# Kernel tuning notes

Measured on AMD Instinct MI355X. Metric: run time of the kernel, lower is better.

Reference implementation:

```python
import jax, jax.numpy as jnp
import numpy as np

EPS = 1e-8
TEMP = 0.1

def setup_inputs() -> dict:
    key = jax.random.key(0)
    k1, k2, k3, k4, k5 = jax.random.split(key, 5)
    B, C, S, D = 4096, 1000, 5, 2048
    return {
        "query": jax.random.normal(k1, (B, D), dtype=jnp.float32),
        "labels": jax.random.randint(k2, (B,), 0, C),
        "memory_keys": jax.random.normal(k3, (C, S, D), dtype=jnp.float32),
        "memory_values": jax.random.normal(k4, (C, S, D), dtype=jnp.float32),
        "quality_scores": jax.random.uniform(k5, (C, S), dtype=jnp.float32),
        "top_k": 3,
    }

def reference(query, labels, memory_keys, memory_values, quality_scores, top_k):
    # Gather per-sample class slices: (B, S, D) and (B, S)
    class_keys = memory_keys[labels]
    class_vals = memory_values[labels]
    class_scores = quality_scores[labels]

    # Cosine similarity between query[i] and its class's slot keys
    qn = query / jnp.maximum(jnp.linalg.norm(query, axis=-1, keepdims=True), EPS)
    kn = class_keys / jnp.maximum(jnp.linalg.norm(class_keys, axis=-1, keepdims=True), EPS)
    sim = jnp.einsum('bd,bsd->bs', qn, kn)           # (B, S)
    combined = sim * class_scores                    # (B, S)

    k = min(int(top_k), class_scores.shape[1])
    top_scores, top_idx = jax.lax.top_k(combined, k) # (B, k)
    attn = jax.nn.softmax(top_scores / TEMP, axis=-1)
    top_vals = jnp.take_along_axis(class_vals, top_idx[..., None], axis=1)  # (B, k, D)
    retrieved = jnp.einsum('bk,bkd->bd', attn, top_vals)                    # (B, D)

    # miss handling: classes whose quality scores sum to 0 yield zeros
    hit = class_scores.sum(axis=1) != 0              # (B,)
    retrieved = jnp.where(hit[:, None], retrieved, 0.0)
    weights = jnp.where(hit, top_scores.mean(axis=-1), 0.0)
    return retrieved, weights
```

## Files before the change

kernel.cpp:

```cpp
#include <hip/hip_runtime.h>
#include <math.h>

#define THREADS 256
#define WPB 4
#define NSLOT 5
#define EPSF 1e-8f

template<int N4T>
__global__ __launch_bounds__(THREADS, 4) void mb_wave_kernel(
    const float* __restrict__ query,
    const int*   __restrict__ labels,
    const float* __restrict__ mkeys,
    const float* __restrict__ mvals,
    const float* __restrict__ qscores,
    const int*   __restrict__ topk_p,
    float* __restrict__ out_ret,
    float* __restrict__ out_w,
    int B, int n4_rt)
{
    const int tid  = threadIdx.x;
    const int lane = tid & 63;
    const int wave = tid >> 6;
    const int i    = blockIdx.x * WPB + wave;
    if (i >= B) return;

    const int n4 = (N4T > 0) ? N4T : n4_rt;
    const int c  = labels[i];

    int k = topk_p[0];
    if (k > NSLOT) k = NSLOT;
    if (k < 1) k = 1;

    const float4* q4 = reinterpret_cast<const float4*>(query) + (size_t)i * n4;
    const float4* k4 = reinterpret_cast<const float4*>(mkeys) + (size_t)c * NSLOT * n4;
    const float4* v4 = reinterpret_cast<const float4*>(mvals) + (size_t)c * NSLOT * n4;
    float4*       o4 = reinterpret_cast<float4*>(out_ret) + (size_t)i * n4;

    float qq = 0.f;
    float dot[NSLOT], kk[NSLOT];
#pragma unroll
    for (int s = 0; s < NSLOT; ++s) { dot[s] = 0.f; kk[s] = 0.f; }

    auto body1 = [&](int idx) {
        float4 q = q4[idx];
        qq = fmaf(q.x, q.x, fmaf(q.y, q.y, fmaf(q.z, q.z, fmaf(q.w, q.w, qq))));
#pragma unroll
        for (int s = 0; s < NSLOT; ++s) {
            float4 kv = k4[s * n4 + idx];
            dot[s] = fmaf(q.x, kv.x, fmaf(q.y, kv.y, fmaf(q.z, kv.z, fmaf(q.w, kv.w, dot[s]))));
            kk[s]  = fmaf(kv.x, kv.x, fmaf(kv.y, kv.y, fmaf(kv.z, kv.z, fmaf(kv.w, kv.w, kk[s]))));
        }
    };
    if constexpr (N4T > 0) {
#pragma unroll
        for (int j = 0; j < N4T / 64; ++j) body1(lane + j * 64);
    } else {
        for (int idx = lane; idx < n4; idx += 64) body1(idx);
    }

#pragma unroll
    for (int off = 1; off < 64; off <<= 1) {
        qq += __shfl_xor(qq, off);
#pragma unroll
        for (int s = 0; s < NSLOT; ++s) {
            dot[s] += __shfl_xor(dot[s], off);
            kk[s]  += __shfl_xor(kk[s], off);
        }
    }

    float qn = fmaxf(sqrtf(qq), EPSF);

    float scores[NSLOT];
    float ssum = 0.f;
#pragma unroll
    for (int s = 0; s < NSLOT; ++s) {
        scores[s] = qscores[(size_t)c * NSLOT + s];
        ssum += scores[s];
    }

    float comb[NSLOT];
#pragma unroll
    for (int s = 0; s < NSLOT; ++s) {
        float kn = fmaxf(sqrtf(kk[s]), EPSF);
        comb[s] = (dot[s] / (qn * kn)) * scores[s];
    }

    bool used[NSLOT];
#pragma unroll
    for (int s = 0; s < NSLOT; ++s) used[s] = false;
    float tsc[NSLOT];
    int   tix[NSLOT];
#pragma unroll
    for (int j = 0; j < NSLOT; ++j) {
        if (j < k) {
            float best = -INFINITY;
            int bi = 0;
#pragma unroll
            for (int s = 0; s < NSLOT; ++s) {
                if (!used[s] && comb[s] > best) { best = comb[s]; bi = s; }
            }
            used[bi] = true;
            tsc[j] = best;
            tix[j] = bi;
        }
    }

    const bool hit = (ssum != 0.0f);
    float m = tsc[0];
    float esum = 0.f, wsum = 0.f;
    float a[NSLOT];
#pragma unroll
    for (int j = 0; j < NSLOT; ++j) {
        if (j < k) {
            a[j] = __expf((tsc[j] - m) * 10.0f);
            esum += a[j];
            wsum += tsc[j];
        } else {
            a[j] = 0.f;
        }
    }
    float inv = hit ? (1.0f / esum) : 0.0f;
#pragma unroll
    for (int j = 0; j < NSLOT; ++j) a[j] *= inv;

    if (lane == 0) out_w[i] = hit ? (wsum / (float)k) : 0.0f;

    auto body2 = [&](int idx) {
        float4 acc = make_float4(0.f, 0.f, 0.f, 0.f);
#pragma unroll
        for (int j = 0; j < NSLOT; ++j) {
            if (j < k) {
                float4 v = v4[tix[j] * n4 + idx];
                acc.x = fmaf(a[j], v.x, acc.x);
                acc.y = fmaf(a[j], v.y, acc.y);
                acc.z = fmaf(a[j], v.z, acc.z);
                acc.w = fmaf(a[j], v.w, acc.w);
            }
        }
        o4[idx] = acc;
    };
    if constexpr (N4T > 0) {
#pragma unroll
        for (int j = 0; j < N4T / 64; ++j) body2(lane + j * 64);
    } else {
        for (int idx = lane; idx < n4; idx += 64) body2(idx);
    }
}

extern "C" void kernel_launch(void* const* d_in, const int* in_sizes, int n_in,
                              void* d_out, int out_size, void* d_ws, size_t ws_size,
                              hipStream_t stream) {
    const float* query   = (const float*)d_in[0];
    const int*   labels  = (const int*)d_in[1];
    const float* mkeys   = (const float*)d_in[2];
    const float* mvals   = (const float*)d_in[3];
    const float* qscores = (const float*)d_in[4];
    const int*   topk    = (const int*)d_in[5];

    const int B  = in_sizes[1];
    const int D  = in_sizes[0] / B;
    const int n4 = D >> 2;

    float* out_ret = (float*)d_out;
    float* out_w   = out_ret + (size_t)B * D;

    dim3 grid((B + WPB - 1) / WPB), block(THREADS);
    if (D == 2048) {
        mb_wave_kernel<512><<<grid, block, 0, stream>>>(
            query, labels, mkeys, mvals, qscores, topk, out_ret, out_w, B, n4);
    } else if (D == 1024) {
        mb_wave_kernel<256><<<grid, block, 0, stream>>>(
            query, labels, mkeys, mvals, qscores, topk, out_ret, out_w, B, n4);
    } else {
        mb_wave_kernel<0><<<grid, block, 0, stream>>>(
            query, labels, mkeys, mvals, qscores, topk, out_ret, out_w, B, n4);
    }
}
```

Measured before the change: 49.93 us.

## Software-pipeline key/value loads, use dense slot weights, one wave per block

Restructures the kernel to launch one 64-thread block per query row and adds explicit 3-deep register prefetch of query/key chunks and of value chunks. The top-k attention weights are scattered into a dense per-slot weight vector, so the value phase reads all five slots unconditionally instead of branching on the selected indices. Query loads and output stores use nontemporal hints. This aims to raise memory-level parallelism and remove divergent indexed loads, at the cost of reading two extra value slots per row and higher register pressure.

```diff
diff --git a/kernel.cpp b/kernel.cpp
--- a/kernel.cpp
+++ b/kernel.cpp
@@ -1,13 +1,14 @@
 #include <hip/hip_runtime.h>
 #include <math.h>
 
-#define THREADS 256
-#define WPB 4
 #define NSLOT 5
+#define NBUF 3
 #define EPSF 1e-8f
 
-template<int N4T>
-__global__ __launch_bounds__(THREADS, 4) void mb_wave_kernel(
+typedef float f4 __attribute__((ext_vector_type(4)));
+
+template<int N4>
+__global__ __launch_bounds__(64, 4) void mb_kernel(
     const float* __restrict__ query,
     const int*   __restrict__ labels,
     const float* __restrict__ mkeys,
@@ -18,44 +19,70 @@
     float* __restrict__ out_w,
     int B, int n4_rt)
 {
-    const int tid  = threadIdx.x;
-    const int lane = tid & 63;
-    const int wave = tid >> 6;
-    const int i    = blockIdx.x * WPB + wave;
+    const int lane = threadIdx.x;
+    const int i    = blockIdx.x;
     if (i >= B) return;
-
-    const int n4 = (N4T > 0) ? N4T : n4_rt;
-    const int c  = labels[i];
+    const int c = labels[i];
 
     int k = topk_p[0];
     if (k > NSLOT) k = NSLOT;
     if (k < 1) k = 1;
 
-    const float4* q4 = reinterpret_cast<const float4*>(query) + (size_t)i * n4;
-    const float4* k4 = reinterpret_cast<const float4*>(mkeys) + (size_t)c * NSLOT * n4;
-    const float4* v4 = reinterpret_cast<const float4*>(mvals) + (size_t)c * NSLOT * n4;
-    float4*       o4 = reinterpret_cast<float4*>(out_ret) + (size_t)i * n4;
+    const int n4 = (N4 > 0) ? N4 : n4_rt;
+    const f4* q4 = reinterpret_cast<const f4*>(query) + (size_t)i * n4;
+    const f4* k4 = reinterpret_cast<const f4*>(mkeys) + (size_t)c * NSLOT * n4;
+    const f4* v4 = reinterpret_cast<const f4*>(mvals) + (size_t)c * NSLOT * n4;
+    f4*       o4 = reinterpret_cast<f4*>(out_ret) + (size_t)i * n4;
 
     float qq = 0.f;
     float dot[NSLOT], kk[NSLOT];
 #pragma unroll
     for (int s = 0; s < NSLOT; ++s) { dot[s] = 0.f; kk[s] = 0.f; }
 
-    auto body1 = [&](int idx) {
-        float4 q = q4[idx];
-        qq = fmaf(q.x, q.x, fmaf(q.y, q.y, fmaf(q.z, q.z, fmaf(q.w, q.w, qq))));
-#pragma unroll
-        for (int s = 0; s < NSLOT; ++s) {
-            float4 kv = k4[s * n4 + idx];
-            dot[s] = fmaf(q.x, kv.x, fmaf(q.y, kv.y, fmaf(q.z, kv.z, fmaf(q.w, kv.w, dot[s]))));
-            kk[s]  = fmaf(kv.x, kv.x, fmaf(kv.y, kv.y, fmaf(kv.z, kv.z, fmaf(kv.w, kv.w, kk[s]))));
-        }
-    };
-    if constexpr (N4T > 0) {
-#pragma unroll
-        for (int j = 0; j < N4T / 64; ++j) body1(lane + j * 64);
+    if constexpr (N4 > 0) {
+        constexpr int NCH = N4 / 64;
+        f4 qb[NBUF];
+        f4 kb[NBUF][NSLOT];
+#pragma unroll
+        for (int b = 0; b < NBUF; ++b) {
+            qb[b] = __builtin_nontemporal_load(&q4[lane + b * 64]);
+#pragma unroll
+            for (int s = 0; s < NSLOT; ++s)
+                kb[b][s] = k4[s * N4 + lane + b * 64];
+        }
+#pragma unroll
+        for (int j = 0; j < NCH; ++j) {
+            constexpr int M = NBUF;
+            const int b = j % M;
+            f4 q = qb[b];
+            f4 kv[NSLOT];
+#pragma unroll
+            for (int s = 0; s < NSLOT; ++s) kv[s] = kb[b][s];
+            if (j + M < NCH) {
+                qb[b] = __builtin_nontemporal_load(&q4[lane + (j + M) * 64]);
+#pragma unroll
+                for (int s = 0; s < NSLOT; ++s)
+                    kb[b][s] = k4[s * N4 + lane + (j + M) * 64];
+            }
+            qq = fmaf(q.x, q.x, fmaf(q.y, q.y, fmaf(q.z, q.z, fmaf(q.w, q.w, qq))));
+#pragma unroll
+            for (int s = 0; s < NSLOT; ++s) {
+                dot[s] = fmaf(q.x, kv[s].x, fmaf(q.y, kv[s].y,
+                         fmaf(q.z, kv[s].z, fmaf(q.w, kv[s].w, dot[s]))));
+                kk[s]  = fmaf(kv[s].x, kv[s].x, fmaf(kv[s].y, kv[s].y,
+                         fmaf(kv[s].z, kv[s].z, fmaf(kv[s].w, kv[s].w, kk[s]))));
+            }
+        }
     } else {
-        for (int idx = lane; idx < n4; idx += 64) body1(idx);
+        for (int idx = lane; idx < n4; idx += 64) {
+            f4 q = q4[idx];
+            qq = fmaf(q.x, q.x, fmaf(q.y, q.y, fmaf(q.z, q.z, fmaf(q.w, q.w, qq))));
+            for (int s = 0; s < NSLOT; ++s) {
+                f4 kv = k4[s * n4 + idx];
+                dot[s] = fmaf(q.x, kv.x, fmaf(q.y, kv.y, fmaf(q.z, kv.z, fmaf(q.w, kv.w, dot[s]))));
+                kk[s]  = fmaf(kv.x, kv.x, fmaf(kv.y, kv.y, fmaf(kv.z, kv.z, fmaf(kv.w, kv.w, kk[s]))));
+            }
+        }
     }
 
 #pragma unroll
@@ -92,17 +119,18 @@
     int   tix[NSLOT];
 #pragma unroll
     for (int j = 0; j < NSLOT; ++j) {
+        float best = -INFINITY;
+        int bi = 0;
         if (j < k) {
-            float best = -INFINITY;
-            int bi = 0;
 #pragma unroll
             for (int s = 0; s < NSLOT; ++s) {
                 if (!used[s] && comb[s] > best) { best = comb[s]; bi = s; }
             }
-            used[bi] = true;
-            tsc[j] = best;
-            tix[j] = bi;
-        }
+#pragma unroll
+            for (int s = 0; s < NSLOT; ++s) used[s] = used[s] || (s == bi);
+        }
+        tsc[j] = best;
+        tix[j] = bi;
     }
 
     const bool hit = (ssum != 0.0f);
@@ -120,30 +148,61 @@
         }
     }
     float inv = hit ? (1.0f / esum) : 0.0f;
-#pragma unroll
-    for (int j = 0; j < NSLOT; ++j) a[j] *= inv;
+
+    float w[NSLOT];
+#pragma unroll
+    for (int s = 0; s < NSLOT; ++s) {
+        float ws = 0.f;
+#pragma unroll
+        for (int j = 0; j < NSLOT; ++j)
+            if (j < k && tix[j] == s) ws += a[j] * inv;
+        w[s] = ws;
+    }
 
     if (lane == 0) out_w[i] = hit ? (wsum / (float)k) : 0.0f;
 
-    auto body2 = [&](int idx) {
-        float4 acc = make_float4(0.f, 0.f, 0.f, 0.f);
-#pragma unroll
-        for (int j = 0; j < NSLOT; ++j) {
-            if (j < k) {
-                float4 v = v4[tix[j] * n4 + idx];
-                acc.x = fmaf(a[j], v.x, acc.x);
-                acc.y = fmaf(a[j], v.y, acc.y);
-                acc.z = fmaf(a[j], v.z, acc.z);
-                acc.w = fmaf(a[j], v.w, acc.w);
-            }
-        }
-        o4[idx] = acc;
-    };
-    if constexpr (N4T > 0) {
-#pragma unroll
-        for (int j = 0; j < N4T / 64; ++j) body2(lane + j * 64);
+    if constexpr (N4 > 0) {
+        constexpr int NCH = N4 / 64;
+        f4 vb[NBUF][NSLOT];
+#pragma unroll
+        for (int b = 0; b < NBUF; ++b)
+#pragma unroll
+            for (int s = 0; s < NSLOT; ++s)
+                vb[b][s] = v4[s * N4 + lane + b * 64];
+#pragma unroll
+        for (int j = 0; j < NCH; ++j) {
+            constexpr int M = NBUF;
+            const int b = j % M;
+            f4 vv[NSLOT];
+#pragma unroll
+            for (int s = 0; s < NSLOT; ++s) vv[s] = vb[b][s];
+            if (j + M < NCH) {
+#pragma unroll
+                for (int s = 0; s < NSLOT; ++s)
+                    vb[b][s] = v4[s * N4 + lane + (j + M) * 64];
+            }
+            f4 acc = (f4)(0.f);
+#pragma unroll
+            for (int s = 0; s < NSLOT; ++s) {
+                acc.x = fmaf(w[s], vv[s].x, acc.x);
+                acc.y = fmaf(w[s], vv[s].y, acc.y);
+                acc.z = fmaf(w[s], vv[s].z, acc.z);
+                acc.w = fmaf(w[s], vv[s].w, acc.w);
+            }
+            __builtin_nontemporal_store(acc, &o4[lane + j * 64]);
+        }
     } else {
-        for (int idx = lane; idx < n4; idx += 64) body2(idx);
+        for (int idx = lane; idx < n4; idx += 64) {
+            f4 acc = (f4)(0.f);
+            for (int s = 0; s < NSLOT; ++s) {
+                f4 v = v4[s * n4 + idx];
+                acc.x = fmaf(w[s], v.x, acc.x);
+                acc.y = fmaf(w[s], v.y, acc.y);
+                acc.z = fmaf(w[s], v.z, acc.z);
+                acc.w = fmaf(w[s], v.w, acc.w);
+            }
+            o4[idx] = acc;
+        }
     }
 }
 
@@ -164,15 +223,15 @@
     float* out_ret = (float*)d_out;
     float* out_w   = out_ret + (size_t)B * D;
 
-    dim3 grid((B + WPB - 1) / WPB), block(THREADS);
+    dim3 grid(B), block(64);
     if (D == 2048) {
-        mb_wave_kernel<512><<<grid, block, 0, stream>>>(
+        mb_kernel<512><<<grid, block, 0, stream>>>(
             query, labels, mkeys, mvals, qscores, topk, out_ret, out_w, B, n4);
     } else if (D == 1024) {
-        mb_wave_kernel<256><<<grid, block, 0, stream>>>(
+        mb_kernel<256><<<grid, block, 0, stream>>>(
             query, labels, mkeys, mvals, qscores, topk, out_ret, out_w, B, n4);
     } else {
-        mb_wave_kernel<0><<<grid, block, 0, stream>>>(
+        mb_kernel<0><<<grid, block, 0, stream>>>(
             query, labels, mkeys, mvals, qscores, topk, out_ret, out_w, B, n4);
     }
 }
```

Result: slower. 57.23 us (+14.6%).

## Software-pipeline key/value loads with inline asm and explicit waitcnt per wave

Applied to the files above, without the earlier changes.

Replaces the 4-wave block kernel with one 64-lane block per sample. Key and value loads go through a hand-scheduled triple-buffered pipeline of inline-asm global_load_dwordx4 with explicit s_waitcnt, and the first value loads are issued before the reduction and top-k so they overlap that latency. Value accumulation now reads all 5 slots with a per-slot weight (zero for unselected), which removes data-dependent indexing but adds loads of values that are never weighted. It also adds large register pressure and relies on hand-counted vmcnt values.

```diff
diff --git a/kernel.cpp b/kernel.cpp
--- a/kernel.cpp
+++ b/kernel.cpp
@@ -1,13 +1,61 @@
 #include <hip/hip_runtime.h>
 #include <math.h>
 
-#define THREADS 256
-#define WPB 4
 #define NSLOT 5
 #define EPSF 1e-8f
 
-template<int N4T>
-__global__ __launch_bounds__(THREADS, 4) void mb_wave_kernel(
+typedef float f4 __attribute__((ext_vector_type(4)));
+
+#define GLOAD(dst, ptr) \
+    asm volatile("global_load_dwordx4 %0, %1, off" : "=v"(dst) : "v"(ptr) : "memory")
+
+#define WAITCNT(n) do { \
+    asm volatile("s_waitcnt vmcnt(" #n ")" ::: "memory"); \
+    __builtin_amdgcn_sched_barrier(0); \
+} while (0)
+
+#define ISSUE_K(b, j) do { \
+    GLOAD(qb[b],    qp  + (j) * 64); \
+    GLOAD(kb[b][0], kp0 + (j) * 64); \
+    GLOAD(kb[b][1], kp1 + (j) * 64); \
+    GLOAD(kb[b][2], kp2 + (j) * 64); \
+    GLOAD(kb[b][3], kp3 + (j) * 64); \
+    GLOAD(kb[b][4], kp4 + (j) * 64); \
+} while (0)
+
+#define DOT1(s, t) do { \
+    dot[s] = fmaf(q.x, t.x, fmaf(q.y, t.y, fmaf(q.z, t.z, fmaf(q.w, t.w, dot[s])))); \
+    kk[s]  = fmaf(t.x, t.x, fmaf(t.y, t.y, fmaf(t.z, t.z, fmaf(t.w, t.w, kk[s])))); \
+} while (0)
+
+#define CONSUME_K(b) do { \
+    f4 q = qb[b]; \
+    qq = fmaf(q.x, q.x, fmaf(q.y, q.y, fmaf(q.z, q.z, fmaf(q.w, q.w, qq)))); \
+    { f4 t = kb[b][0]; DOT1(0, t); } \
+    { f4 t = kb[b][1]; DOT1(1, t); } \
+    { f4 t = kb[b][2]; DOT1(2, t); } \
+    { f4 t = kb[b][3]; DOT1(3, t); } \
+    { f4 t = kb[b][4]; DOT1(4, t); } \
+} while (0)
+
+#define ISSUE_V(b, m) do { \
+    GLOAD(vb[b][0], vp0 + (m) * 64); \
+    GLOAD(vb[b][1], vp1 + (m) * 64); \
+    GLOAD(vb[b][2], vp2 + (m) * 64); \
+    GLOAD(vb[b][3], vp3 + (m) * 64); \
+    GLOAD(vb[b][4], vp4 + (m) * 64); \
+} while (0)
+
+#define CONSUME_V(b, m) do { \
+    f4 acc = vb[b][0] * w0; \
+    acc += vb[b][1] * w1; \
+    acc += vb[b][2] * w2; \
+    acc += vb[b][3] * w3; \
+    acc += vb[b][4] * w4; \
+    op[(m) * 64] = acc; \
+} while (0)
+
+__global__ __launch_bounds__(64, 3) void mb_pipe_kernel(
     const float* __restrict__ query,
     const int*   __restrict__ labels,
     const float* __restrict__ mkeys,
@@ -16,47 +64,60 @@
     const int*   __restrict__ topk_p,
     float* __restrict__ out_ret,
     float* __restrict__ out_w,
-    int B, int n4_rt)
+    int B)
 {
-    const int tid  = threadIdx.x;
-    const int lane = tid & 63;
-    const int wave = tid >> 6;
-    const int i    = blockIdx.x * WPB + wave;
+    const int lane = threadIdx.x;
+    const int i    = blockIdx.x;
     if (i >= B) return;
 
-    const int n4 = (N4T > 0) ? N4T : n4_rt;
-    const int c  = labels[i];
-
+    const int c = labels[i];
     int k = topk_p[0];
     if (k > NSLOT) k = NSLOT;
     if (k < 1) k = 1;
 
-    const float4* q4 = reinterpret_cast<const float4*>(query) + (size_t)i * n4;
-    const float4* k4 = reinterpret_cast<const float4*>(mkeys) + (size_t)c * NSLOT * n4;
-    const float4* v4 = reinterpret_cast<const float4*>(mvals) + (size_t)c * NSLOT * n4;
-    float4*       o4 = reinterpret_cast<float4*>(out_ret) + (size_t)i * n4;
+    float sc0 = qscores[(size_t)c * NSLOT + 0];
+    float sc1 = qscores[(size_t)c * NSLOT + 1];
+    float sc2 = qscores[(size_t)c * NSLOT + 2];
+    float sc3 = qscores[(size_t)c * NSLOT + 3];
+    float sc4 = qscores[(size_t)c * NSLOT + 4];
+    asm volatile("" : "+v"(sc0), "+v"(sc1), "+v"(sc2), "+v"(sc3), "+v"(sc4));
+
+    const int n4 = 512;
+    const f4* q4 = reinterpret_cast<const f4*>(query) + (size_t)i * n4;
+    const f4* k4 = reinterpret_cast<const f4*>(mkeys) + (size_t)c * NSLOT * n4;
+    const f4* v4 = reinterpret_cast<const f4*>(mvals) + (size_t)c * NSLOT * n4;
+    f4*       o4 = reinterpret_cast<f4*>(out_ret) + (size_t)i * n4;
+
+    const f4* qp  = q4 + lane;
+    const f4* kp0 = k4 + lane;
+    const f4* kp1 = k4 + 512 + lane;
+    const f4* kp2 = k4 + 1024 + lane;
+    const f4* kp3 = k4 + 1536 + lane;
+    const f4* kp4 = k4 + 2048 + lane;
+    const f4* vp0 = v4 + lane;
+    const f4* vp1 = v4 + 512 + lane;
+    const f4* vp2 = v4 + 1024 + lane;
+    const f4* vp3 = v4 + 1536 + lane;
+    const f4* vp4 = v4 + 2048 + lane;
+    f4*       op  = o4 + lane;
 
     float qq = 0.f;
-    float dot[NSLOT], kk[NSLOT];
-#pragma unroll
-    for (int s = 0; s < NSLOT; ++s) { dot[s] = 0.f; kk[s] = 0.f; }
-
-    auto body1 = [&](int idx) {
-        float4 q = q4[idx];
-        qq = fmaf(q.x, q.x, fmaf(q.y, q.y, fmaf(q.z, q.z, fmaf(q.w, q.w, qq))));
-#pragma unroll
-        for (int s = 0; s < NSLOT; ++s) {
-            float4 kv = k4[s * n4 + idx];
-            dot[s] = fmaf(q.x, kv.x, fmaf(q.y, kv.y, fmaf(q.z, kv.z, fmaf(q.w, kv.w, dot[s]))));
-            kk[s]  = fmaf(kv.x, kv.x, fmaf(kv.y, kv.y, fmaf(kv.z, kv.z, fmaf(kv.w, kv.w, kk[s]))));
-        }
-    };
-    if constexpr (N4T > 0) {
-#pragma unroll
-        for (int j = 0; j < N4T / 64; ++j) body1(lane + j * 64);
-    } else {
-        for (int idx = lane; idx < n4; idx += 64) body1(idx);
-    }
+    float dot[NSLOT] = {0.f, 0.f, 0.f, 0.f, 0.f};
+    float kk[NSLOT]  = {0.f, 0.f, 0.f, 0.f, 0.f};
+
+    f4 qb[3];
+    f4 kb[3][NSLOT];
+    f4 vb[3][NSLOT];
+
+    ISSUE_K(0, 0); ISSUE_K(1, 1); ISSUE_K(2, 2);
+    WAITCNT(12); CONSUME_K(0); ISSUE_K(0, 3);
+    WAITCNT(12); CONSUME_K(1); ISSUE_K(1, 4);
+    WAITCNT(12); CONSUME_K(2); ISSUE_K(2, 5);
+    WAITCNT(12); CONSUME_K(0); ISSUE_K(0, 6);
+    WAITCNT(12); CONSUME_K(1); ISSUE_K(1, 7);
+    WAITCNT(12); CONSUME_K(2); ISSUE_V(0, 0);
+    WAITCNT(11); CONSUME_K(0); ISSUE_V(1, 1);
+    WAITCNT(10); CONSUME_K(1); ISSUE_V(2, 2);
 
 #pragma unroll
     for (int off = 1; off < 64; off <<= 1) {
@@ -69,20 +130,14 @@
     }
 
     float qn = fmaxf(sqrtf(qq), EPSF);
-
-    float scores[NSLOT];
-    float ssum = 0.f;
-#pragma unroll
-    for (int s = 0; s < NSLOT; ++s) {
-        scores[s] = qscores[(size_t)c * NSLOT + s];
-        ssum += scores[s];
-    }
+    float scr[NSLOT] = {sc0, sc1, sc2, sc3, sc4};
+    float ssum = sc0 + sc1 + sc2 + sc3 + sc4;
 
     float comb[NSLOT];
 #pragma unroll
     for (int s = 0; s < NSLOT; ++s) {
         float kn = fmaxf(sqrtf(kk[s]), EPSF);
-        comb[s] = (dot[s] / (qn * kn)) * scores[s];
+        comb[s] = (dot[s] / (qn * kn)) * scr[s];
     }
 
     bool used[NSLOT];
@@ -92,17 +147,18 @@
     int   tix[NSLOT];
 #pragma unroll
     for (int j = 0; j < NSLOT; ++j) {
+        float best = -INFINITY;
+        int bi = 0;
         if (j < k) {
-            float best = -INFINITY;
-            int bi = 0;
 #pragma unroll
             for (int s = 0; s < NSLOT; ++s) {
                 if (!used[s] && comb[s] > best) { best = comb[s]; bi = s; }
             }
-            used[bi] = true;
-            tsc[j] = best;
-            tix[j] = bi;
-        }
+#pragma unroll
+            for (int s = 0; s < NSLOT; ++s) used[s] = used[s] || (s == bi);
+        }
+        tsc[j] = best;
+        tix[j] = bi;
     }
 
     const bool hit = (ssum != 0.0f);
@@ -120,30 +176,109 @@
         }
     }
     float inv = hit ? (1.0f / esum) : 0.0f;
-#pragma unroll
-    for (int j = 0; j < NSLOT; ++j) a[j] *= inv;
+
+    float wgt[NSLOT];
+#pragma unroll
+    for (int s = 0; s < NSLOT; ++s) {
+        float ws = 0.f;
+#pragma unroll
+        for (int j = 0; j < NSLOT; ++j)
+            if (j < k && tix[j] == s) ws += a[j] * inv;
+        wgt[s] = ws;
+    }
+    const float w0 = wgt[0], w1 = wgt[1], w2 = wgt[2], w3 = wgt[3], w4 = wgt[4];
 
     if (lane == 0) out_w[i] = hit ? (wsum / (float)k) : 0.0f;
 
-    auto body2 = [&](int idx) {
-        float4 acc = make_float4(0.f, 0.f, 0.f, 0.f);
-#pragma unroll
-        for (int j = 0; j < NSLOT; ++j) {
-            if (j < k) {
-                float4 v = v4[tix[j] * n4 + idx];
-                acc.x = fmaf(a[j], v.x, acc.x);
-                acc.y = fmaf(a[j], v.y, acc.y);
-                acc.z = fmaf(a[j], v.z, acc.z);
-                acc.w = fmaf(a[j], v.w, acc.w);
-            }
+    WAITCNT(10); CONSUME_V(0, 0); ISSUE_V(0, 3);
+    WAITCNT(10); CONSUME_V(1, 1); ISSUE_V(1, 4);
+    WAITCNT(10); CONSUME_V(2, 2); ISSUE_V(2, 5);
+    WAITCNT(10); CONSUME_V(0, 3); ISSUE_V(0, 6);
+    WAITCNT(10); CONSUME_V(1, 4); ISSUE_V(1, 7);
+    WAITCNT(10); CONSUME_V(2, 5);
+    WAITCNT(5);  CONSUME_V(0, 6);
+    WAITCNT(0);  CONSUME_V(1, 7);
+}
+
+__global__ __launch_bounds__(64) void mb_generic_kernel(
+    const float* __restrict__ query,
+    const int*   __restrict__ labels,
+    const float* __restrict__ mkeys,
+    const float* __restrict__ mvals,
+    const float* __restrict__ qscores,
+    const int*   __restrict__ topk_p,
+    float* __restrict__ out_ret,
+    float* __restrict__ out_w,
+    int B, int n4)
+{
+    const int lane = threadIdx.x;
+    const int i    = blockIdx.x;
+    if (i >= B) return;
+    const int c = labels[i];
+    int k = topk_p[0];
+    if (k > NSLOT) k = NSLOT;
+    if (k < 1) k = 1;
+
+    const f4* q4 = reinterpret_cast<const f4*>(query) + (size_t)i * n4;
+    const f4* k4 = reinterpret_cast<const f4*>(mkeys) + (size_t)c * NSLOT * n4;
+    const f4* v4 = reinterpret_cast<const f4*>(mvals) + (size_t)c * NSLOT * n4;
+    f4*       o4 = reinterpret_cast<f4*>(out_ret) + (size_t)i * n4;
+
+    float qq = 0.f, dot[NSLOT] = {0}, kk[NSLOT] = {0};
+    for (int idx = lane; idx < n4; idx += 64) {
+        f4 q = q4[idx];
+        qq = fmaf(q.x, q.x, fmaf(q.y, q.y, fmaf(q.z, q.z, fmaf(q.w, q.w, qq))));
+        for (int s = 0; s < NSLOT; ++s) {
+            f4 t = k4[s * n4 + idx];
+            dot[s] = fmaf(q.x, t.x, fmaf(q.y, t.y, fmaf(q.z, t.z, fmaf(q.w, t.w, dot[s]))));
+            kk[s]  = fmaf(t.x, t.x, fmaf(t.y, t.y, fmaf(t.z, t.z, fmaf(t.w, t.w, kk[s]))));
+        }
+    }
+    for (int off = 1; off < 64; off <<= 1) {
+        qq += __shfl_xor(qq, off);
+        for (int s = 0; s < NSLOT; ++s) {
+            dot[s] += __shfl_xor(dot[s], off);
+            kk[s]  += __shfl_xor(kk[s], off);
+        }
+    }
+    float qn = fmaxf(sqrtf(qq), EPSF);
+    float scr[NSLOT], ssum = 0.f;
+    for (int s = 0; s < NSLOT; ++s) { scr[s] = qscores[(size_t)c * NSLOT + s]; ssum += scr[s]; }
+    float comb[NSLOT];
+    for (int s = 0; s < NSLOT; ++s)
+        comb[s] = (dot[s] / (qn * fmaxf(sqrtf(kk[s]), EPSF))) * scr[s];
+    bool used[NSLOT] = {false, false, false, false, false};
+    float tsc[NSLOT]; int tix[NSLOT];
+    for (int j = 0; j < NSLOT; ++j) {
+        float best = -INFINITY; int bi = 0;
+        if (j < k) {
+            for (int s = 0; s < NSLOT; ++s)
+                if (!used[s] && comb[s] > best) { best = comb[s]; bi = s; }
+            used[bi] = true;
+        }
+        tsc[j] = best; tix[j] = bi;
+    }
+    const bool hit = (ssum != 0.0f);
+    float m = tsc[0], esum = 0.f, wsum = 0.f, a[NSLOT];
+    for (int j = 0; j < NSLOT; ++j) {
+        if (j < k) { a[j] = __expf((tsc[j] - m) * 10.0f); esum += a[j]; wsum += tsc[j]; }
+        else a[j] = 0.f;
+    }
+    float inv = hit ? (1.0f / esum) : 0.0f;
+    float w[NSLOT];
+    for (int s = 0; s < NSLOT; ++s) {
+        float ws = 0.f;
+        for (int j = 0; j < NSLOT; ++j) if (j < k && tix[j] == s) ws += a[j] * inv;
+        w[s] = ws;
+    }
+    if (lane == 0) out_w[i] = hit ? (wsum / (float)k) : 0.0f;
+    for (int idx = lane; idx < n4; idx += 64) {
+        f4 acc = (f4)(0.f);
+        for (int s = 0; s < NSLOT; ++s) {
+            f4 v = v4[s * n4 + idx];
+            acc += v * w[s];
         }
         o4[idx] = acc;
-    };
-    if constexpr (N4T > 0) {
-#pragma unroll
-        for (int j = 0; j < N4T / 64; ++j) body2(lane + j * 64);
-    } else {
-        for (int idx = lane; idx < n4; idx += 64) body2(idx);
     }
 }
 
@@ -164,15 +299,11 @@
     float* out_ret = (float*)d_out;
     float* out_w   = out_ret + (size_t)B * D;
 
-    dim3 grid((B + WPB - 1) / WPB), block(THREADS);
     if (D == 2048) {
-        mb_wave_kernel<512><<<grid, block, 0, stream>>>(
+        mb_pipe_kernel<<<dim3(B), dim3(64), 0, stream>>>(
+            query, labels, mkeys, mvals, qscores, topk, out_ret, out_w, B);
+    } else {
+        mb_generic_kernel<<<dim3(B), dim3(64), 0, stream>>>(
             query, labels, mkeys, mvals, qscores, topk, out_ret, out_w, B, n4);
-    } else if (D == 1024) {
-        mb_wave_kernel<256><<<grid, block, 0, stream>>>(
-            query, labels, mkeys, mvals, qscores, topk, out_ret, out_w, B, n4);
-    } else {
-        mb_wave_kernel<0><<<grid, block, 0, stream>>>(
-            query, labels, mkeys, mvals, qscores, topk, out_ret, out_w, B, n4);
     }
 }
```

Result: slower. 59.87 us (+19.9%).

## Bucket queries by class label to improve key/value cache reuse

Applied to the files above, without the earlier changes.

Adds histogram, scan and scatter kernels that sort query indices by label, so waves processing the same class run close together and share key/value slices in cache. Blocks are striped across 8 groups, presumably to spread the work over XCDs. The value pass now reads all 5 slots with per-slot weights, dropping the data-dependent indexed gather at the cost of reading extra value rows. This adds three small launches plus a memset, and the per-wave output writes become scattered.

```diff
diff --git a/kernel.cpp b/kernel.cpp
--- a/kernel.cpp
+++ b/kernel.cpp
@@ -1,19 +1,61 @@
 #include <hip/hip_runtime.h>
 #include <math.h>
 
-#define THREADS 256
-#define WPB 4
 #define NSLOT 5
 #define EPSF 1e-8f
+#define WPB 4
+
+typedef float f4 __attribute__((ext_vector_type(4)));
+
+
+__global__ void hist_kernel(const int* __restrict__ labels, int* __restrict__ counts, int B) {
+    int i = blockIdx.x * blockDim.x + threadIdx.x;
+    if (i < B) atomicAdd(&counts[labels[i]], 1);
+}
+
+__global__ void scan_kernel(const int* __restrict__ counts, int* __restrict__ cursor, int C) {
+    __shared__ int sh[1024];
+    __shared__ int running;
+    if (threadIdx.x == 0) running = 0;
+    __syncthreads();
+    for (int base = 0; base < C; base += 1024) {
+        int t = base + threadIdx.x;
+        int v = (t < C) ? counts[t] : 0;
+        sh[threadIdx.x] = v;
+        __syncthreads();
+        for (int d = 1; d < 1024; d <<= 1) {
+            int x = (threadIdx.x >= d) ? sh[threadIdx.x - d] : 0;
+            __syncthreads();
+            sh[threadIdx.x] += x;
+            __syncthreads();
+        }
+        int excl = sh[threadIdx.x] - v + running;
+        if (t < C) cursor[t] = excl;
+        __syncthreads();
+        if (threadIdx.x == 0) running += sh[1023];
+        __syncthreads();
+    }
+}
+
+__global__ void scatter_kernel(const int* __restrict__ labels, int* __restrict__ cursor,
+                               int* __restrict__ bucket, int B) {
+    int i = blockIdx.x * blockDim.x + threadIdx.x;
+    if (i < B) {
+        int slot = atomicAdd(&cursor[labels[i]], 1);
+        bucket[slot] = i;
+    }
+}
+
 
 template<int N4T>
-__global__ __launch_bounds__(THREADS, 4) void mb_wave_kernel(
+__global__ __launch_bounds__(64 * WPB, 4) void mb_wave_kernel(
     const float* __restrict__ query,
-    const int*   __restrict__ labels,
     const float* __restrict__ mkeys,
     const float* __restrict__ mvals,
     const float* __restrict__ qscores,
     const int*   __restrict__ topk_p,
+    const int*   __restrict__ labels,
+    const int*   __restrict__ bucket,
     float* __restrict__ out_ret,
     float* __restrict__ out_w,
     int B, int n4_rt)
@@ -21,41 +63,42 @@
     const int tid  = threadIdx.x;
     const int lane = tid & 63;
     const int wave = tid >> 6;
-    const int i    = blockIdx.x * WPB + wave;
-    if (i >= B) return;
-
-    const int n4 = (N4T > 0) ? N4T : n4_rt;
-    const int c  = labels[i];
+
+    int j;
+    if (bucket) {
+        const int stripe = B >> 3;
+        j = (blockIdx.x & 7) * stripe + (blockIdx.x >> 3) * WPB + wave;
+    } else {
+        j = blockIdx.x * WPB + wave;
+    }
+    if (j >= B) return;
+    const int i = bucket ? bucket[j] : j;
+    const int c = labels[i];
 
     int k = topk_p[0];
     if (k > NSLOT) k = NSLOT;
     if (k < 1) k = 1;
 
-    const float4* q4 = reinterpret_cast<const float4*>(query) + (size_t)i * n4;
-    const float4* k4 = reinterpret_cast<const float4*>(mkeys) + (size_t)c * NSLOT * n4;
-    const float4* v4 = reinterpret_cast<const float4*>(mvals) + (size_t)c * NSLOT * n4;
-    float4*       o4 = reinterpret_cast<float4*>(out_ret) + (size_t)i * n4;
+    const int n4 = (N4T > 0) ? N4T : n4_rt;
+    const f4* q4 = reinterpret_cast<const f4*>(query) + (size_t)i * n4;
+    const f4* k4 = reinterpret_cast<const f4*>(mkeys) + (size_t)c * NSLOT * n4;
+    const f4* v4 = reinterpret_cast<const f4*>(mvals) + (size_t)c * NSLOT * n4;
+    f4*       o4 = reinterpret_cast<f4*>(out_ret) + (size_t)i * n4;
 
     float qq = 0.f;
     float dot[NSLOT], kk[NSLOT];
 #pragma unroll
     for (int s = 0; s < NSLOT; ++s) { dot[s] = 0.f; kk[s] = 0.f; }
 
-    auto body1 = [&](int idx) {
-        float4 q = q4[idx];
+    for (int idx = lane; idx < n4; idx += 64) {
+        f4 q = q4[idx];
         qq = fmaf(q.x, q.x, fmaf(q.y, q.y, fmaf(q.z, q.z, fmaf(q.w, q.w, qq))));
 #pragma unroll
         for (int s = 0; s < NSLOT; ++s) {
-            float4 kv = k4[s * n4 + idx];
+            f4 kv = k4[s * n4 + idx];
             dot[s] = fmaf(q.x, kv.x, fmaf(q.y, kv.y, fmaf(q.z, kv.z, fmaf(q.w, kv.w, dot[s]))));
             kk[s]  = fmaf(kv.x, kv.x, fmaf(kv.y, kv.y, fmaf(kv.z, kv.z, fmaf(kv.w, kv.w, kk[s]))));
         }
-    };
-    if constexpr (N4T > 0) {
-#pragma unroll
-        for (int j = 0; j < N4T / 64; ++j) body1(lane + j * 64);
-    } else {
-        for (int idx = lane; idx < n4; idx += 64) body1(idx);
     }
 
 #pragma unroll
@@ -70,19 +113,19 @@
 
     float qn = fmaxf(sqrtf(qq), EPSF);
 
-    float scores[NSLOT];
+    float scr[NSLOT];
     float ssum = 0.f;
 #pragma unroll
     for (int s = 0; s < NSLOT; ++s) {
-        scores[s] = qscores[(size_t)c * NSLOT + s];
-        ssum += scores[s];
+        scr[s] = qscores[(size_t)c * NSLOT + s];
+        ssum += scr[s];
     }
 
     float comb[NSLOT];
 #pragma unroll
     for (int s = 0; s < NSLOT; ++s) {
         float kn = fmaxf(sqrtf(kk[s]), EPSF);
-        comb[s] = (dot[s] / (qn * kn)) * scores[s];
+        comb[s] = (dot[s] / (qn * kn)) * scr[s];
     }
 
     bool used[NSLOT];
@@ -91,18 +134,19 @@
     float tsc[NSLOT];
     int   tix[NSLOT];
 #pragma unroll
-    for (int j = 0; j < NSLOT; ++j) {
-        if (j < k) {
-            float best = -INFINITY;
-            int bi = 0;
+    for (int jj = 0; jj < NSLOT; ++jj) {
+        float best = -INFINITY;
+        int bi = 0;
+        if (jj < k) {
 #pragma unroll
             for (int s = 0; s < NSLOT; ++s) {
                 if (!used[s] && comb[s] > best) { best = comb[s]; bi = s; }
             }
-            used[bi] = true;
-            tsc[j] = best;
-            tix[j] = bi;
-        }
+#pragma unroll
+            for (int s = 0; s < NSLOT; ++s) used[s] = used[s] || (s == bi);
+        }
+        tsc[jj] = best;
+        tix[jj] = bi;
     }
 
     const bool hit = (ssum != 0.0f);
@@ -110,40 +154,40 @@
     float esum = 0.f, wsum = 0.f;
     float a[NSLOT];
 #pragma unroll
-    for (int j = 0; j < NSLOT; ++j) {
-        if (j < k) {
-            a[j] = __expf((tsc[j] - m) * 10.0f);
-            esum += a[j];
-            wsum += tsc[j];
+    for (int jj = 0; jj < NSLOT; ++jj) {
+        if (jj < k) {
+            a[jj] = __expf((tsc[jj] - m) * 10.0f);
+            esum += a[jj];
+            wsum += tsc[jj];
         } else {
-            a[j] = 0.f;
+            a[jj] = 0.f;
         }
     }
     float inv = hit ? (1.0f / esum) : 0.0f;
-#pragma unroll
-    for (int j = 0; j < NSLOT; ++j) a[j] *= inv;
+
+    float wgt[NSLOT];
+#pragma unroll
+    for (int s = 0; s < NSLOT; ++s) {
+        float ws = 0.f;
+#pragma unroll
+        for (int jj = 0; jj < NSLOT; ++jj)
+            if (jj < k && tix[jj] == s) ws += a[jj] * inv;
+        wgt[s] = ws;
+    }
 
     if (lane == 0) out_w[i] = hit ? (wsum / (float)k) : 0.0f;
 
-    auto body2 = [&](int idx) {
-        float4 acc = make_float4(0.f, 0.f, 0.f, 0.f);
-#pragma unroll
-        for (int j = 0; j < NSLOT; ++j) {
-            if (j < k) {
-                float4 v = v4[tix[j] * n4 + idx];
-                acc.x = fmaf(a[j], v.x, acc.x);
-                acc.y = fmaf(a[j], v.y, acc.y);
-                acc.z = fmaf(a[j], v.z, acc.z);
-                acc.w = fmaf(a[j], v.w, acc.w);
-            }
+    for (int idx = lane; idx < n4; idx += 64) {
+        f4 acc = (f4)(0.f);
+#pragma unroll
+        for (int s = 0; s < NSLOT; ++s) {
+            f4 v = v4[s * n4 + idx];
+            acc.x = fmaf(wgt[s], v.x, acc.x);
+            acc.y = fmaf(wgt[s], v.y, acc.y);
+            acc.z = fmaf(wgt[s], v.z, acc.z);
+            acc.w = fmaf(wgt[s], v.w, acc.w);
         }
         o4[idx] = acc;
-    };
-    if constexpr (N4T > 0) {
-#pragma unroll
-        for (int j = 0; j < N4T / 64; ++j) body2(lane + j * 64);
-    } else {
-        for (int idx = lane; idx < n4; idx += 64) body2(idx);
     }
 }
 
@@ -160,19 +204,34 @@
     const int B  = in_sizes[1];
     const int D  = in_sizes[0] / B;
     const int n4 = D >> 2;
+    const int C  = in_sizes[4] / NSLOT;
 
     float* out_ret = (float*)d_out;
     float* out_w   = out_ret + (size_t)B * D;
 
-    dim3 grid((B + WPB - 1) / WPB), block(THREADS);
+    const bool can_bin = (B % 32 == 0) &&
+                         ((size_t)(2 * C + B) * sizeof(int) <= ws_size);
+
+    const int* bucket = nullptr;
+    if (can_bin) {
+        int* counts = (int*)d_ws;
+        int* bkt    = counts + 2 * C;
+        hipMemsetAsync(counts, 0, (size_t)C * sizeof(int), stream);
+        hist_kernel<<<dim3((B + 255) / 256), dim3(256), 0, stream>>>(labels, counts, B);
+        scan_kernel<<<dim3(1), dim3(1024), 0, stream>>>(counts, counts + C, C);
+        scatter_kernel<<<dim3((B + 255) / 256), dim3(256), 0, stream>>>(labels, counts + C, bkt, B);
+        bucket = bkt;
+    }
+
+    dim3 grid((B + WPB - 1) / WPB), block(64 * WPB);
     if (D == 2048) {
         mb_wave_kernel<512><<<grid, block, 0, stream>>>(
-            query, labels, mkeys, mvals, qscores, topk, out_ret, out_w, B, n4);
+            query, mkeys, mvals, qscores, topk, labels, bucket, out_ret, out_w, B, n4);
     } else if (D == 1024) {
         mb_wave_kernel<256><<<grid, block, 0, stream>>>(
-            query, labels, mkeys, mvals, qscores, topk, out_ret, out_w, B, n4);
+            query, mkeys, mvals, qscores, topk, labels, bucket, out_ret, out_w, B, n4);
     } else {
         mb_wave_kernel<0><<<grid, block, 0, stream>>>(
-            query, labels, mkeys, mvals, qscores, topk, out_ret, out_w, B, n4);
-    }
-}
+            query, mkeys, mvals, qscores, topk, labels, bucket, out_ret, out_w, B, n4);
+    }
+}
```

After: 40.42 us. 19.0% less time.
